# Optimization experiments

Measured on AMD Instinct MI355X. Metric: run time of the kernel, lower is better.

Reference implementation:

```python
import jax, jax.numpy as jnp
import numpy as np

H = 1024      # hidden_size
NH = 16       # num_attention_heads
HD = H // NH  # attention_head_size = 64
B, S = 2, 2048


def setup_inputs() -> dict:
    key = jax.random.key(0)
    ks = jax.random.split(key, 8)
    scale = 1.0 / np.sqrt(H)
    return {
        "hidden_states": jax.random.normal(ks[0], (B, S, H), dtype=jnp.float32),
        "attention_mask": jnp.zeros((B, 1, 1, S), dtype=jnp.float32),
        "Wq": jax.random.normal(ks[1], (H, H), dtype=jnp.float32) * scale,
        "bq": jax.random.normal(ks[2], (H,), dtype=jnp.float32) * 0.02,
        "Wk": jax.random.normal(ks[3], (H, H), dtype=jnp.float32) * scale,
        "bk": jax.random.normal(ks[4], (H,), dtype=jnp.float32) * 0.02,
        "Wv": jax.random.normal(ks[5], (H, H), dtype=jnp.float32) * scale,
        "bv": jax.random.normal(ks[6], (H,), dtype=jnp.float32) * 0.02,
    }


def _split_heads(x):
    # [B,S,H] -> [B,NH,S,HD]
    b, s, _ = x.shape
    return x.reshape(b, s, NH, HD).transpose(0, 2, 1, 3)


def reference(hidden_states, attention_mask, Wq, bq, Wk, bk, Wv, bv):
    q = _split_heads(hidden_states @ Wq.T + bq)  # [B,NH,S,HD]
    k = _split_heads(hidden_states @ Wk.T + bk)
    v = _split_heads(hidden_states @ Wv.T + bv)
    scores = jnp.einsum("bhqd,bhkd->bhqk", q, k) / np.sqrt(HD).astype(np.float32)
    scores = scores + attention_mask  # additive mask, broadcast over heads/queries
    weights = jax.nn.softmax(scores, axis=-1)  # dropout is identity in eval mode
    ctx = jnp.einsum("bhqk,bhkd->bhqd", weights, v)  # [B,NH,S,HD]
    return ctx.transpose(0, 2, 1, 3).reshape(hidden_states.shape[0], hidden_states.shape[1], H)
```

## Files before the change

### kernel.cpp

```cpp
#include <hip/hip_runtime.h>
#include <hip/hip_bf16.h>
#include <math.h>

#define HSZ   1024
#define NHEAD 16
#define HDIM  64
#define BATCH 2
#define SEQ   2048

#define LOG2E 1.4426950408889634f

typedef __attribute__((ext_vector_type(8))) short short8;
typedef __attribute__((ext_vector_type(4))) short short4_t;
typedef __attribute__((ext_vector_type(4))) float floatx4;

typedef __attribute__((address_space(1))) const unsigned int gu32;
typedef __attribute__((address_space(3))) unsigned int lu32;

__device__ __forceinline__ void g2lds16(const void* g, void* l) {
    __builtin_amdgcn_global_load_lds((gu32*)g, (lu32*)l, 16, 0, 0);
}

__device__ __forceinline__ short f2bf(float f) {
    union { float f; unsigned u; } v; v.f = f;
    unsigned r = (v.u + 0x7FFF + ((v.u >> 16) & 1)) >> 16;
    return (short)r;
}

__device__ __forceinline__ unsigned pk2(float a, float b) {
    __hip_bfloat162 h = __float22bfloat162_rn(make_float2(a, b));
    return *(unsigned*)&h;
}

__device__ __forceinline__ float ex2(float x) {
#if __has_builtin(__builtin_amdgcn_exp2f)
    return __builtin_amdgcn_exp2f(x);
#else
    return exp2f(x);
#endif
}

__global__ __launch_bounds__(256) void convert_kernel(
    const float4* __restrict__ X, const float4* __restrict__ Wq,
    const float4* __restrict__ Wk, const float4* __restrict__ Wv,
    const float4* __restrict__ Mask,
    short4_t* __restrict__ Xb, short4_t* __restrict__ Wb,
    float4* __restrict__ Mw)
{
    int idx = blockIdx.x * 256 + threadIdx.x;
    if (idx >= 1835008) {
        int t = idx - 1835008;
        float4 f = Mask[t];
        float4 o;
        o.x = f.x * LOG2E; o.y = f.y * LOG2E;
        o.z = f.z * LOG2E; o.w = f.w * LOG2E;
        Mw[t] = o;
        return;
    }
    const float4* src; short4_t* dst;
    if (idx < 1048576) { src = X + idx; dst = Xb + idx; }
    else {
        int t = idx - 1048576;
        int sel = t >> 18;
        int wi  = t & 0x3FFFF;
        src = (sel == 0 ? Wq : sel == 1 ? Wk : Wv) + wi;
        dst = Wb + (sel << 18) + wi;
    }
    float4 f = *src;
    short4_t o;
    o.x = f2bf(f.x); o.y = f2bf(f.y); o.z = f2bf(f.z); o.w = f2bf(f.w);
    *dst = o;
}

__global__ __launch_bounds__(256, 3) void qkv_mfma_kernel(
    const short* __restrict__ Xb, const short* __restrict__ Wb,
    const float* __restrict__ bq, const float* __restrict__ bk,
    const float* __restrict__ bv,
    short* __restrict__ qo, short* __restrict__ ko, short* __restrict__ vT)
{
    __shared__ short Sm[128 * 132];
    short* As = Sm;
    short* Bs = Sm + 8192;

    const int tid  = threadIdx.x;
    const int lane = tid & 63;
    const int w    = tid >> 6;
    const int l    = lane & 15, quad = lane >> 4;
    const int gM   = blockIdx.y * 128;
    const int gN   = blockIdx.x * 128;
    const int wm   = (w >> 1) * 64, wn = (w & 1) * 64;
    const int ci   = lane >> 3, pb = lane & 7;

    floatx4 acc[4][4] = {};

    for (int kt = 0; kt < HSZ / 64; ++kt) {
        const int k0 = kt * 64;
        __syncthreads();
        #pragma unroll
        for (int u = 0; u < 4; ++u) {
            int c  = w * 4 + u;
            int r  = c * 8 + ci;
            int lb = pb ^ (r & 7);
            g2lds16(Xb + (size_t)(gM + r) * HSZ + k0 + lb * 8, &As[c * 512]);
            g2lds16(Wb + (size_t)(gN + r) * HSZ + k0 + lb * 8, &Bs[c * 512]);
        }
        __syncthreads();
        #pragma unroll
        for (int kk = 0; kk < 2; ++kk) {
            short8 a[4], b[4];
            #pragma unroll
            for (int i = 0; i < 4; ++i) {
                int m = wm + i * 16 + l;
                a[i] = *(const short8*)&As[m * 64 + (((quad + kk * 4) ^ (m & 7)) << 3)];
                int n = wn + i * 16 + l;
                b[i] = *(const short8*)&Bs[n * 64 + (((quad + kk * 4) ^ (n & 7)) << 3)];
            }
            #pragma unroll
            for (int i = 0; i < 4; ++i)
                #pragma unroll
                for (int j = 0; j < 4; ++j)
                    acc[i][j] = __builtin_amdgcn_mfma_f32_16x16x32_bf16(
                        a[i], b[j], acc[i][j], 0, 0, 0);
        }
    }

    const int mat = gN >> 10;

    if (mat == 2) {
        __syncthreads();
        #pragma unroll
        for (int j = 0; j < 4; ++j) {
            int fl = wn + j * 16 + l;
            float bv_ = bv[(gN & 1023) + fl];
            #pragma unroll
            for (int i = 0; i < 4; ++i)
                #pragma unroll
                for (int r = 0; r < 4; ++r)
                    Sm[fl * 132 + wm + i * 16 + quad * 4 + r]
                        = f2bf(acc[i][j][r] + bv_);
        }
        __syncthreads();
        const int bb = gM >> 11, ss0 = gM & (SEQ - 1);
        #pragma unroll
        for (int it = 0; it < 16; ++it) {
            int f = (tid >> 5) + it * 8;
            int c = (tid & 31) * 4;
            short4_t val = *(const short4_t*)&Sm[f * 132 + c];
            int nft = (gN & 1023) + f;
            int head = nft >> 6, d = nft & 63;
            *(short4_t*)&vT[(((size_t)(bb * NHEAD + head)) * HDIM + d) * SEQ
                            + ss0 + c] = val;
        }
        return;
    }

    const float* bias = (mat == 0) ? bq : bk;
    short* dst        = (mat == 0) ? qo : ko;
    const float qscale = (mat == 0) ? 0.125f * LOG2E : 1.0f;

    #pragma unroll
    for (int j = 0; j < 4; ++j) {
        int nft = (gN & 1023) + wn + j * 16 + l;
        float bv_ = bias[nft];
        int head = nft >> 6, d = nft & 63;
        #pragma unroll
        for (int i = 0; i < 4; ++i) {
            #pragma unroll
            for (int r = 0; r < 4; ++r) {
                int gr = gM + wm + i * 16 + quad * 4 + r;
                int bb = gr >> 11, ss = gr & (SEQ - 1);
                float val = (acc[i][j][r] + bv_) * qscale;
                dst[((((size_t)bb * NHEAD + head) * SEQ + ss) << 6) + d] = f2bf(val);
            }
        }
    }
}

__global__ __launch_bounds__(256, 2) void attn_kernel(
    const short* __restrict__ Qg, const short* __restrict__ Kg,
    const short* __restrict__ VTg, const float* __restrict__ maskw,
    float* __restrict__ out)
{
    __shared__ short Qs[128 * 64];
    __shared__ short Ks[2][64 * 64];
    __shared__ short Vt[2][64 * 64];
    __shared__ alignas(16) float Ms[2][64];

    const int tid  = threadIdx.x;
    const int lane = tid & 63;
    const int w    = tid >> 6;
    const int l    = lane & 15, quad = lane >> 4;
    const int qt   = blockIdx.x;
    const int bh   = blockIdx.y;
    const int batch = bh >> 4, head = bh & 15;
    const int ci = lane >> 3, pb = lane & 7;

    const short* Qb = Qg + ((size_t)bh * SEQ + qt * 128) * HDIM;
    const short* Kb = Kg + (size_t)bh * SEQ * HDIM;
    const short* Vb = VTg + (size_t)bh * HDIM * SEQ;
    const float* mrow = maskw + (size_t)batch * SEQ;

    #pragma unroll
    for (int u = 0; u < 4; ++u) {
        int c = w * 4 + u;
        int r = c * 8 + ci;
        int lb = pb ^ (r & 7);
        g2lds16(Qb + (size_t)r * HDIM + lb * 8, &Qs[c * 512]);
    }
    #pragma unroll
    for (int u = 0; u < 2; ++u) {
        int c = w * 2 + u;
        int r = c * 8 + ci;
        int lb = pb ^ (r & 7);
        g2lds16(Kb + (size_t)r * HDIM + lb * 8, &Ks[0][c * 512]);
        g2lds16(Vb + (size_t)r * SEQ + lb * 8, &Vt[0][c * 512]);
    }
    if (tid < 16) g2lds16(mrow + tid * 4, &Ms[0][0]);
    __syncthreads();

    short8 aq[2][2];
    #pragma unroll
    for (int i = 0; i < 2; ++i)
        #pragma unroll
        for (int kk = 0; kk < 2; ++kk) {
            int m = w * 32 + i * 16 + l;
            aq[i][kk] = *(const short8*)&Qs[m * 64 + (((quad + kk * 4) ^ (m & 7)) << 3)];
        }

    floatx4 o[2][4] = {};
    float l_i[2] = {0.f, 0.f};
    const int psw = (l & 7) << 1;

    for (int kt = 0; kt < SEQ / 64; ++kt) {
        const int cur = kt & 1, nxt = cur ^ 1;
        if (kt + 1 < SEQ / 64) {
            const int r0 = (kt + 1) * 64;
            #pragma unroll
            for (int u = 0; u < 2; ++u) {
                int c = w * 2 + u;
                int r = c * 8 + ci;
                int lb = pb ^ (r & 7);
                g2lds16(Kb + (size_t)(r0 + r) * HDIM + lb * 8, &Ks[nxt][c * 512]);
                g2lds16(Vb + (size_t)r * SEQ + r0 + lb * 8, &Vt[nxt][c * 512]);
            }
            if (tid < 16) g2lds16(mrow + r0 + tid * 4, &Ms[nxt][0]);
        }

        float4 mq[4];
        #pragma unroll
        for (int n = 0; n < 4; ++n)
            mq[n] = *(const float4*)&Ms[cur][n * 16 + quad * 4];

        floatx4 s[2][4];
        #pragma unroll
        for (int i = 0; i < 2; ++i)
            #pragma unroll
            for (int n = 0; n < 4; ++n) {
                floatx4 init = {mq[n].x, mq[n].y, mq[n].z, mq[n].w};
                s[i][n] = init;
            }
        #pragma unroll
        for (int kk = 0; kk < 2; ++kk) {
            short8 ak[4];
            #pragma unroll
            for (int n = 0; n < 4; ++n) {
                int kr = n * 16 + l;
                ak[n] = *(const short8*)&Ks[cur][kr * 64 + (((quad + kk * 4) ^ (kr & 7)) << 3)];
            }
            #pragma unroll
            for (int n = 0; n < 4; ++n)
                #pragma unroll
                for (int i = 0; i < 2; ++i)
                    s[i][n] = __builtin_amdgcn_mfma_f32_16x16x32_bf16(
                        ak[n], aq[i][kk], s[i][n], 0, 0, 0);
        }

        #pragma unroll
        for (int i = 0; i < 2; ++i) {
            float rs = 0.f;
            #pragma unroll
            for (int n = 0; n < 4; ++n) {
                s[i][n][0] = ex2(s[i][n][0]);
                s[i][n][1] = ex2(s[i][n][1]);
                s[i][n][2] = ex2(s[i][n][2]);
                s[i][n][3] = ex2(s[i][n][3]);
                rs += (s[i][n][0] + s[i][n][1]) + (s[i][n][2] + s[i][n][3]);
            }
            rs += __shfl_xor(rs, 16);
            rs += __shfl_xor(rs, 32);
            l_i[i] += rs;

            short* Pw = &Qs[(w * 32 + i * 16) * 64];
            #pragma unroll
            for (int n = 0; n < 4; ++n) {
                int kb = n * 4 + quad;
                unsigned u0 = pk2(s[i][n][0], s[i][n][1]);
                unsigned u1 = pk2(s[i][n][2], s[i][n][3]);
                *(uint2*)&Pw[l * 64 + ((kb ^ psw) << 2)] = make_uint2(u0, u1);
            }
        }

        #pragma unroll
        for (int kk = 0; kk < 2; ++kk) {
            short8 bvf[4], ap[2];
            #pragma unroll
            for (int n = 0; n < 4; ++n) {
                int d = n * 16 + l;
                bvf[n] = *(const short8*)&Vt[cur][d * 64 + (((quad + kk * 4) ^ (d & 7)) << 3)];
            }
            #pragma unroll
            for (int i = 0; i < 2; ++i) {
                const short* Pw = &Qs[(w * 32 + i * 16) * 64];
                ap[i] = *(const short8*)&Pw[l * 64 + (((quad * 2 + kk * 8) ^ psw) << 2)];
            }
            #pragma unroll
            for (int i = 0; i < 2; ++i)
                #pragma unroll
                for (int n = 0; n < 4; ++n)
                    o[i][n] = __builtin_amdgcn_mfma_f32_16x16x32_bf16(
                        ap[i], bvf[n], o[i][n], 0, 0, 0);
        }
        __syncthreads();
    }

    #pragma unroll
    for (int i = 0; i < 2; ++i) {
        #pragma unroll
        for (int r = 0; r < 4; ++r) {
            float inv = 1.0f / __shfl(l_i[i], (lane & 48) + ((lane >> 4) << 2) + r);
            int qrow = qt * 128 + w * 32 + i * 16 + quad * 4 + r;
            #pragma unroll
            for (int n = 0; n < 4; ++n)
                out[((size_t)batch * SEQ + qrow) * HSZ + head * HDIM + n * 16 + l]
                    = o[i][n][r] * inv;
        }
    }
}

extern "C" void kernel_launch(void* const* d_in, const int* in_sizes, int n_in,
                              void* d_out, int out_size, void* d_ws, size_t ws_size,
                              hipStream_t stream) {
    const float* hs   = (const float*)d_in[0];
    const float* mask = (const float*)d_in[1];
    const float* Wq   = (const float*)d_in[2];
    const float* bq   = (const float*)d_in[3];
    const float* Wk   = (const float*)d_in[4];
    const float* bk   = (const float*)d_in[5];
    const float* Wv   = (const float*)d_in[6];
    const float* bv   = (const float*)d_in[7];
    float* out = (float*)d_out;

    short* Xb = (short*)d_ws;
    short* Wb = Xb + 4194304;
    short* qb = Wb + 3145728;
    short* kb = qb + 4194304;
    short* vT = kb + 4194304;
    float* Mw = (float*)(vT + 4194304);

    convert_kernel<<<7172, 256, 0, stream>>>(
        (const float4*)hs, (const float4*)Wq, (const float4*)Wk, (const float4*)Wv,
        (const float4*)mask, (short4_t*)Xb, (short4_t*)Wb, (float4*)Mw);

    dim3 g2(3 * HSZ / 128, BATCH * SEQ / 128);
    qkv_mfma_kernel<<<g2, 256, 0, stream>>>(Xb, Wb, bq, bk, bv, qb, kb, vT);

    dim3 g4(SEQ / 128, BATCH * NHEAD);
    attn_kernel<<<g4, 256, 0, stream>>>(qb, kb, vT, Mw, out);
}
```

Measured before the change: 168.4 us.

## Split attention waves across key halves and feed P from registers

The attention kernel now lays its four waves out as 2 query-halves by 2 key-halves. The S^T accumulators are packed straight into bf16 A-operands for the PV MFMA, which removes the P round-trip through LDS and its read-back. The V^T store in the projection kernel is permuted so the register layout of P matches the K dimension of V. The two key-half partial outputs and row sums are combined through LDS at the end, which adds an epilogue reduction and extra LDS use. The grid is also flattened so that consecutive blocks share a query tile across heads.

```diff
diff --git a/kernel.cpp b/kernel.cpp
--- a/kernel.cpp
+++ b/kernel.cpp
@@ -146,10 +146,12 @@
             int f = (tid >> 5) + it * 8;
             int c = (tid & 31) * 4;
             short4_t val = *(const short4_t*)&Sm[f * 132 + c];
+            int b = (c >> 2) & 15;
+            int cp = (c & ~63) | ((((b & 8) | ((b & 3) << 1) | ((b >> 2) & 1))) << 2);
             int nft = (gN & 1023) + f;
             int head = nft >> 6, d = nft & 63;
             *(short4_t*)&vT[(((size_t)(bb * NHEAD + head)) * HDIM + d) * SEQ
-                            + ss0 + c] = val;
+                            + ss0 + cp] = val;
         }
         return;
     }
@@ -182,17 +184,20 @@
     float* __restrict__ out)
 {
     __shared__ short Qs[128 * 64];
-    __shared__ short Ks[2][64 * 64];
-    __shared__ short Vt[2][64 * 64];
+    __shared__ alignas(16) short Ks[2][64 * 64];
+    __shared__ alignas(16) short Vt[2][64 * 64];
     __shared__ alignas(16) float Ms[2][64];
+    __shared__ alignas(16) float Lx[2][4][64];
 
     const int tid  = threadIdx.x;
     const int lane = tid & 63;
     const int w    = tid >> 6;
     const int l    = lane & 15, quad = lane >> 4;
-    const int qt   = blockIdx.x;
-    const int bh   = blockIdx.y;
+    const int idx  = blockIdx.x;
+    const int bh   = idx & 31;
+    const int qt   = idx >> 5;
     const int batch = bh >> 4, head = bh & 15;
+    const int qh = w & 1, kh = w >> 1;
     const int ci = lane >> 3, pb = lane & 7;
 
     const short* Qb = Qg + ((size_t)bh * SEQ + qt * 128) * HDIM;
@@ -218,18 +223,17 @@
     if (tid < 16) g2lds16(mrow + tid * 4, &Ms[0][0]);
     __syncthreads();
 
-    short8 aq[2][2];
+    short8 aq[4][2];
     #pragma unroll
-    for (int i = 0; i < 2; ++i)
+    for (int n = 0; n < 4; ++n)
         #pragma unroll
         for (int kk = 0; kk < 2; ++kk) {
-            int m = w * 32 + i * 16 + l;
-            aq[i][kk] = *(const short8*)&Qs[m * 64 + (((quad + kk * 4) ^ (m & 7)) << 3)];
-        }
-
-    floatx4 o[2][4] = {};
-    float l_i[2] = {0.f, 0.f};
-    const int psw = (l & 7) << 1;
+            int m = qh * 64 + n * 16 + l;
+            aq[n][kk] = *(const short8*)&Qs[m * 64 + (((quad + kk * 4) ^ (m & 7)) << 3)];
+        }
+
+    floatx4 o[4][4] = {};
+    float l_i[4] = {0.f, 0.f, 0.f, 0.f};
 
     for (int kt = 0; kt < SEQ / 64; ++kt) {
         const int cur = kt & 1, nxt = cur ^ 1;
@@ -246,93 +250,110 @@
             if (tid < 16) g2lds16(mrow + r0 + tid * 4, &Ms[nxt][0]);
         }
 
-        float4 mq[4];
-        #pragma unroll
-        for (int n = 0; n < 4; ++n)
-            mq[n] = *(const float4*)&Ms[cur][n * 16 + quad * 4];
+        float4 mq[2];
+        #pragma unroll
+        for (int m = 0; m < 2; ++m)
+            mq[m] = *(const float4*)&Ms[cur][kh * 32 + m * 16 + quad * 4];
 
         floatx4 s[2][4];
         #pragma unroll
-        for (int i = 0; i < 2; ++i)
-            #pragma unroll
-            for (int n = 0; n < 4; ++n) {
-                floatx4 init = {mq[n].x, mq[n].y, mq[n].z, mq[n].w};
-                s[i][n] = init;
-            }
+        for (int m = 0; m < 2; ++m) {
+            floatx4 ini = {mq[m].x, mq[m].y, mq[m].z, mq[m].w};
+            #pragma unroll
+            for (int n = 0; n < 4; ++n) s[m][n] = ini;
+        }
         #pragma unroll
         for (int kk = 0; kk < 2; ++kk) {
-            short8 ak[4];
-            #pragma unroll
-            for (int n = 0; n < 4; ++n) {
-                int kr = n * 16 + l;
-                ak[n] = *(const short8*)&Ks[cur][kr * 64 + (((quad + kk * 4) ^ (kr & 7)) << 3)];
-            }
-            #pragma unroll
-            for (int n = 0; n < 4; ++n)
-                #pragma unroll
-                for (int i = 0; i < 2; ++i)
-                    s[i][n] = __builtin_amdgcn_mfma_f32_16x16x32_bf16(
-                        ak[n], aq[i][kk], s[i][n], 0, 0, 0);
-        }
-
-        #pragma unroll
-        for (int i = 0; i < 2; ++i) {
-            float rs = 0.f;
-            #pragma unroll
-            for (int n = 0; n < 4; ++n) {
-                s[i][n][0] = ex2(s[i][n][0]);
-                s[i][n][1] = ex2(s[i][n][1]);
-                s[i][n][2] = ex2(s[i][n][2]);
-                s[i][n][3] = ex2(s[i][n][3]);
-                rs += (s[i][n][0] + s[i][n][1]) + (s[i][n][2] + s[i][n][3]);
-            }
-            rs += __shfl_xor(rs, 16);
-            rs += __shfl_xor(rs, 32);
-            l_i[i] += rs;
-
-            short* Pw = &Qs[(w * 32 + i * 16) * 64];
-            #pragma unroll
-            for (int n = 0; n < 4; ++n) {
-                int kb = n * 4 + quad;
-                unsigned u0 = pk2(s[i][n][0], s[i][n][1]);
-                unsigned u1 = pk2(s[i][n][2], s[i][n][3]);
-                *(uint2*)&Pw[l * 64 + ((kb ^ psw) << 2)] = make_uint2(u0, u1);
-            }
-        }
-
-        #pragma unroll
-        for (int kk = 0; kk < 2; ++kk) {
-            short8 bvf[4], ap[2];
-            #pragma unroll
-            for (int n = 0; n < 4; ++n) {
-                int d = n * 16 + l;
-                bvf[n] = *(const short8*)&Vt[cur][d * 64 + (((quad + kk * 4) ^ (d & 7)) << 3)];
-            }
-            #pragma unroll
-            for (int i = 0; i < 2; ++i) {
-                const short* Pw = &Qs[(w * 32 + i * 16) * 64];
-                ap[i] = *(const short8*)&Pw[l * 64 + (((quad * 2 + kk * 8) ^ psw) << 2)];
-            }
-            #pragma unroll
-            for (int i = 0; i < 2; ++i)
+            short8 ak[2];
+            #pragma unroll
+            for (int m = 0; m < 2; ++m) {
+                int kr = kh * 32 + m * 16 + l;
+                ak[m] = *(const short8*)&Ks[cur][kr * 64 + (((quad + kk * 4) ^ (kr & 7)) << 3)];
+            }
+            #pragma unroll
+            for (int m = 0; m < 2; ++m)
                 #pragma unroll
                 for (int n = 0; n < 4; ++n)
-                    o[i][n] = __builtin_amdgcn_mfma_f32_16x16x32_bf16(
-                        ap[i], bvf[n], o[i][n], 0, 0, 0);
-        }
-        __syncthreads();
-    }
-
-    #pragma unroll
-    for (int i = 0; i < 2; ++i) {
-        #pragma unroll
-        for (int r = 0; r < 4; ++r) {
-            float inv = 1.0f / __shfl(l_i[i], (lane & 48) + ((lane >> 4) << 2) + r);
-            int qrow = qt * 128 + w * 32 + i * 16 + quad * 4 + r;
-            #pragma unroll
-            for (int n = 0; n < 4; ++n)
-                out[((size_t)batch * SEQ + qrow) * HSZ + head * HDIM + n * 16 + l]
-                    = o[i][n][r] * inv;
+                    s[m][n] = __builtin_amdgcn_mfma_f32_16x16x32_bf16(
+                        ak[m], aq[n][kk], s[m][n], 0, 0, 0);
+        }
+
+        #pragma unroll
+        for (int n = 0; n < 4; ++n) {
+            float rs = 0.f;
+            #pragma unroll
+            for (int m = 0; m < 2; ++m) {
+                s[m][n][0] = ex2(s[m][n][0]);
+                s[m][n][1] = ex2(s[m][n][1]);
+                s[m][n][2] = ex2(s[m][n][2]);
+                s[m][n][3] = ex2(s[m][n][3]);
+                rs += (s[m][n][0] + s[m][n][1]) + (s[m][n][2] + s[m][n][3]);
+            }
+            l_i[n] += rs;
+        }
+
+        short8 ap[4];
+        #pragma unroll
+        for (int n = 0; n < 4; ++n) {
+            union { unsigned u[4]; short8 s8; } pu;
+            pu.u[0] = pk2(s[0][n][0], s[0][n][1]);
+            pu.u[1] = pk2(s[0][n][2], s[0][n][3]);
+            pu.u[2] = pk2(s[1][n][0], s[1][n][1]);
+            pu.u[3] = pk2(s[1][n][2], s[1][n][3]);
+            ap[n] = pu.s8;
+        }
+
+        short8 bvf[4];
+        #pragma unroll
+        for (int nd = 0; nd < 4; ++nd) {
+            int d = nd * 16 + l;
+            bvf[nd] = *(const short8*)&Vt[cur][d * 64 + (((kh * 4 + quad) ^ (d & 7)) << 3)];
+        }
+        #pragma unroll
+        for (int nq = 0; nq < 4; ++nq)
+            #pragma unroll
+            for (int nd = 0; nd < 4; ++nd)
+                o[nq][nd] = __builtin_amdgcn_mfma_f32_16x16x32_bf16(
+                    ap[nq], bvf[nd], o[nq][nd], 0, 0, 0);
+
+        __syncthreads();
+    }
+
+    float* reg = (qh == 0) ? (float*)&Ks[0][0] : (float*)&Vt[0][0];
+    if (kh == 1) {
+        #pragma unroll
+        for (int nq = 0; nq < 4; ++nq)
+            #pragma unroll
+            for (int nd = 0; nd < 4; ++nd)
+                *(floatx4*)&reg[((nq * 4 + nd) * 64 + lane) * 4] = o[nq][nd];
+        #pragma unroll
+        for (int n = 0; n < 4; ++n) Lx[qh][n][lane] = l_i[n];
+    }
+    __syncthreads();
+    if (kh == 0) {
+        #pragma unroll
+        for (int nq = 0; nq < 4; ++nq)
+            #pragma unroll
+            for (int nd = 0; nd < 4; ++nd)
+                o[nq][nd] += *(const floatx4*)&reg[((nq * 4 + nd) * 64 + lane) * 4];
+        #pragma unroll
+        for (int n = 0; n < 4; ++n) {
+            float t = l_i[n] + Lx[qh][n][lane];
+            t += __shfl_xor(t, 16);
+            t += __shfl_xor(t, 32);
+            l_i[n] = t;
+        }
+        #pragma unroll
+        for (int nq = 0; nq < 4; ++nq) {
+            #pragma unroll
+            for (int r = 0; r < 4; ++r) {
+                float inv = 1.0f / __shfl(l_i[nq], (lane & 48) + quad * 4 + r);
+                int qrow = qt * 128 + qh * 64 + nq * 16 + quad * 4 + r;
+                #pragma unroll
+                for (int nd = 0; nd < 4; ++nd)
+                    out[((size_t)batch * SEQ + qrow) * HSZ + head * HDIM + nd * 16 + l]
+                        = o[nq][nd][r] * inv;
+            }
         }
     }
 }
@@ -364,6 +385,5 @@
     dim3 g2(3 * HSZ / 128, BATCH * SEQ / 128);
     qkv_mfma_kernel<<<g2, 256, 0, stream>>>(Xb, Wb, bq, bk, bv, qb, kb, vT);
 
-    dim3 g4(SEQ / 128, BATCH * NHEAD);
-    attn_kernel<<<g4, 256, 0, stream>>>(qb, kb, vT, Mw, out);
-}
+    attn_kernel<<<512, 256, 0, stream>>>(qb, kb, vT, Mw, out);
+}
```

Result: faster. 153.6 us (-8.8%).
